# Performance work log

Measured on AMD Instinct MI355X. Metric: run time of the kernel, lower is better.

## Reference

```python
import jax, jax.numpy as jnp
import numpy as np

N = 20000
E = 320000
IN_CH = 512
OUT_CH = 256


def setup_inputs() -> dict:
    key = jax.random.key(0)
    ks = jax.random.split(key, 24)
    p = lambda k, shape: jax.random.normal(k, shape, jnp.float32) * 0.05
    return {
        "x": jax.random.normal(ks[0], (N, IN_CH), jnp.float32),
        "edge_index": jax.random.randint(ks[1], (2, E), 0, N),
        "original_size": 16384,
        "W1": p(ks[2], (IN_CH, 4 * 256)), "as1": p(ks[3], (4, 256)), "ad1": p(ks[4], (4, 256)), "b1": p(ks[5], (1024,)),
        "lw1": p(ks[6], (IN_CH, 1024)), "lb1": p(ks[7], (1024,)),
        "W2": p(ks[8], (1024, 4 * 256)), "as2": p(ks[9], (4, 256)), "ad2": p(ks[10], (4, 256)), "b2": p(ks[11], (1024,)),
        "lw2": p(ks[12], (1024, 1024)), "lb2": p(ks[13], (1024,)),
        "W3": p(ks[14], (1024, 6 * 256)), "as3": p(ks[15], (6, 256)), "ad3": p(ks[16], (6, 256)), "b3": p(ks[17], (256,)),
        "lw3": p(ks[18], (1024, OUT_CH)), "lb3": p(ks[19], (OUT_CH,)),
    }


def gat_conv(x, src, dst, W, a_src, a_dst, bias, heads, ch, concat):
    """PyG-style GATConv: gather -> edge attention -> segment softmax -> scatter-add."""
    n = x.shape[0]
    h = (x @ W).reshape(n, heads, ch)                      # [N,H,C]
    alpha_s = (h * a_src[None]).sum(-1)                    # [N,H]
    alpha_d = (h * a_dst[None]).sum(-1)                    # [N,H]
    e = jax.nn.leaky_relu(alpha_s[src] + alpha_d[dst], 0.2)  # [E,H]
    m = jax.ops.segment_max(e, dst, num_segments=n)        # per-dst max (stable softmax)
    e = jnp.exp(e - m[dst])
    denom = jax.ops.segment_sum(e, dst, num_segments=n)
    alpha = e / (denom[dst] + 1e-16)                       # [E,H]
    msg = h[src] * alpha[:, :, None]                       # [E,H,C]
    out = jax.ops.segment_sum(msg, dst, num_segments=n)    # [N,H,C]
    out = out.reshape(n, heads * ch) if concat else out.mean(axis=1)
    return out + bias


def reference(x, edge_index, original_size, W1, as1, ad1, b1, lw1, lb1,
              W2, as2, ad2, b2, lw2, lb2, W3, as3, ad3, b3, lw3, lb3):
    n = x.shape[0]
    loops = jnp.arange(n)
    src = jnp.concatenate([edge_index[0], loops])  # PyG add_self_loops=True default
    dst = jnp.concatenate([edge_index[1], loops])
    h = jax.nn.elu(gat_conv(x, src, dst, W1, as1, ad1, b1, 4, 256, True) + x @ lw1 + lb1)
    h = jax.nn.elu(gat_conv(h, src, dst, W2, as2, ad2, b2, 4, 256, True) + h @ lw2 + lb2)
    h = gat_conv(h, src, dst, W3, as3, ad3, b3, 6, 256, False) + h @ lw3 + lb3
    return h[:original_size]
```

## Files before the change

### kernel.cpp

```cpp
#include <hip/hip_runtime.h>

#define N_NODES 20000
#define M_PAD   20096
#define E_EDGES 320000

typedef unsigned short u16;
typedef unsigned int   u32;
typedef __attribute__((ext_vector_type(8))) short bf16x8;
typedef __attribute__((ext_vector_type(4))) float f32x4;

__device__ __forceinline__ float bf2f(u16 u){
  u32 x = ((u32)u) << 16; float f; __builtin_memcpy(&f, &x, 4); return f;
}
__device__ __forceinline__ u16 f2bf(float f){
  u32 u; __builtin_memcpy(&u, &f, 4);
  u += 0x7fffu + ((u >> 16) & 1u);
  return (u16)(u >> 16);
}

__device__ __forceinline__ void gl_lds16(const void* g, void* l){
  __builtin_amdgcn_global_load_lds((const __attribute__((address_space(1))) void*)g,
                                   (__attribute__((address_space(3))) void*)l, 16, 0, 0);
}

__global__ void hist_k(const int* __restrict__ ei, int* __restrict__ cnt){
  int i = blockIdx.x * 256 + threadIdx.x;
  if (i < E_EDGES) atomicAdd(&cnt[ei[E_EDGES + i]], 1);
}

__global__ void scan_k(const int* __restrict__ cnt, int* __restrict__ rowp, int n){
  __shared__ int buf[1024]; __shared__ int carry;
  int tid = threadIdx.x;
  if (tid == 0) carry = 0;
  __syncthreads();
  for (int base = 0; base < n; base += 1024){
    int i = base + tid;
    int v = (i < n) ? cnt[i] : 0;
    buf[tid] = v; __syncthreads();
    for (int off = 1; off < 1024; off <<= 1){
      int t = (tid >= off) ? buf[tid - off] : 0; __syncthreads();
      buf[tid] += t; __syncthreads();
    }
    int incl = buf[tid];
    int c0 = carry;
    __syncthreads();
    if (i < n) rowp[i] = c0 + incl - v;
    if (tid == 1023) carry = c0 + incl;
    __syncthreads();
  }
  if (tid == 0) rowp[n] = carry;
}

__global__ void copy_int_k(const int* __restrict__ a, int* __restrict__ b, int n){
  int i = blockIdx.x * 256 + threadIdx.x; if (i < n) b[i] = a[i];
}

__global__ void scatter_k(const int* __restrict__ ei, int* __restrict__ fill, int* __restrict__ esrc){
  int i = blockIdx.x * 256 + threadIdx.x;
  if (i < E_EDGES){
    int d = ei[E_EDGES + i];
    int p = atomicAdd(&fill[d], 1);
    esrc[p] = ei[i];
  }
}

__global__ void tcast_k(const float* __restrict__ src, int Nc, u16* __restrict__ dst, int n0, int ldd){
  __shared__ float tile[32][33];
  int kb = blockIdx.y * 32, nb = blockIdx.x * 32;
  int tx = threadIdx.x, ty = threadIdx.y;
#pragma unroll
  for (int r = 0; r < 32; r += 8)
    tile[ty + r][tx] = src[(size_t)(kb + ty + r) * Nc + nb + tx];
  __syncthreads();
#pragma unroll
  for (int r = 0; r < 32; r += 8){
    int n = nb + ty + r;
    dst[(size_t)(n0 + n) * ldd + kb + tx] = f2bf(tile[tx][ty + r]);
  }
}

__global__ void castx_k(const float* __restrict__ x, u16* __restrict__ o, int realRows, int cols){
  int r = blockIdx.y, c = blockIdx.x * 256 + threadIdx.x;
  float v = (r < realRows) ? x[(size_t)r * cols + c] : 0.f;
  o[(size_t)r * cols + c] = f2bf(v);
}

__global__ void zpad_k(u16* __restrict__ p, int n){
  int i = blockIdx.x * 256 + threadIdx.x; if (i < n) p[i] = 0;
}

__global__ __launch_bounds__(256)
void gemm_bf16(const u16* __restrict__ A, const u16* __restrict__ Bt, u16* __restrict__ C,
               int N, int K)
{
  __shared__ __attribute__((aligned(16))) u16 lA[128 * 32];
  __shared__ __attribute__((aligned(16))) u16 lB[128 * 32];
  const int tid  = threadIdx.x;
  const int wave = tid >> 6, lane = tid & 63;
  const int bm = blockIdx.x, bn = blockIdx.y;
  const int wm = (wave >> 1) * 64, wn = (wave & 1) * 64;

  const int srow  = wave * 16 + (lane >> 2);
  const int skcol = (lane & 3) * 8;
  const u16* Ag0 = A  + (size_t)(bm * 128 + srow) * K + skcol;
  const u16* Ag1 = Ag0 + (size_t)64 * K;
  const u16* Bg0 = Bt + (size_t)(bn * 128 + srow) * K + skcol;
  const u16* Bg1 = Bg0 + (size_t)64 * K;
  u16* lA0 = lA + wave * 512; u16* lA1 = lA + 2048 + wave * 512;
  u16* lB0 = lB + wave * 512; u16* lB1 = lB + 2048 + wave * 512;

  f32x4 acc[4][4] = {};

  for (int k0 = 0; k0 < K; k0 += 32){
    gl_lds16(Ag0 + k0, lA0);
    gl_lds16(Ag1 + k0, lA1);
    gl_lds16(Bg0 + k0, lB0);
    gl_lds16(Bg1 + k0, lB1);
    __syncthreads();
    const int koff = (lane >> 4) * 8;
    const int rsel = lane & 15;
    bf16x8 af[4], bfr[4];
#pragma unroll
    for (int i = 0; i < 4; i++) af[i]  = *(const bf16x8*)&lA[(wm + i * 16 + rsel) * 32 + koff];
#pragma unroll
    for (int j = 0; j < 4; j++) bfr[j] = *(const bf16x8*)&lB[(wn + j * 16 + rsel) * 32 + koff];
#pragma unroll
    for (int i = 0; i < 4; i++)
#pragma unroll
      for (int j = 0; j < 4; j++)
        acc[i][j] = __builtin_amdgcn_mfma_f32_16x16x32_bf16(af[i], bfr[j], acc[i][j], 0, 0, 0);
    __syncthreads();
  }

  const int r0 = (lane >> 4) * 4, cl = lane & 15;
#pragma unroll
  for (int i = 0; i < 4; i++)
#pragma unroll
    for (int j = 0; j < 4; j++){
      int row = bm * 128 + wm + i * 16 + r0;
      int col = bn * 128 + wn + j * 16 + cl;
      u16* cp = C + (size_t)row * N + col;
#pragma unroll
      for (int r = 0; r < 4; r++) cp[(size_t)r * N] = f2bf(acc[i][j][r]);
    }
}

__global__ void alpha_k(const u16* __restrict__ HG, int ldH,
                        const float* __restrict__ a_s, const float* __restrict__ a_d,
                        float* __restrict__ aS, float* __restrict__ aD, int H)
{
  int n = blockIdx.x, h = blockIdx.y, lane = threadIdx.x;
  const u16* rp = HG + (size_t)n * ldH + h * 256 + lane * 4;
  ushort4 u = *(const ushort4*)rp;
  float4 av = *(const float4*)(a_s + h * 256 + lane * 4);
  float4 dv = *(const float4*)(a_d + h * 256 + lane * 4);
  float x0 = bf2f(u.x), x1 = bf2f(u.y), x2 = bf2f(u.z), x3 = bf2f(u.w);
  float s = x0 * av.x + x1 * av.y + x2 * av.z + x3 * av.w;
  float d = x0 * dv.x + x1 * dv.y + x2 * dv.z + x3 * dv.w;
#pragma unroll
  for (int off = 32; off; off >>= 1){ s += __shfl_down(s, off); d += __shfl_down(d, off); }
  if (lane == 0){ aS[(size_t)n * H + h] = s; aD[(size_t)n * H + h] = d; }
}

template<int H, bool FINAL>
__global__ __launch_bounds__(256)
void agg_k(const u16* __restrict__ HG, int ldH,
           const int* __restrict__ rowp, const int* __restrict__ esrc,
           const float* __restrict__ aS, const float* __restrict__ aD,
           const float* __restrict__ bias, const float* __restrict__ lbias,
           int gatCols, u16* __restrict__ outb, int ldo, float* __restrict__ outf)
{
  constexpr int PERT = H;
  constexpr int MAXE = 256;
  __shared__ float s_m[H], s_dinv[H], s_red[4 * H];
  __shared__ float s_ew[MAXE * H];
  __shared__ float s_fin[FINAL ? 1536 : 4];

  const int dst = blockIdx.x;
  const int tid = threadIdx.x, lane = tid & 63, wv = tid >> 6;
  const int e0 = rowp[dst];
  const int deg = rowp[dst + 1] - e0;
  const int nE = deg + 1;

  float adv[H];
#pragma unroll
  for (int h = 0; h < H; h++) adv[h] = aD[(size_t)dst * H + h];

  float lm[H];
#pragma unroll
  for (int h = 0; h < H; h++) lm[h] = -1e30f;
  for (int i = tid; i < nE; i += 256){
    int s = (i == deg) ? dst : esrc[e0 + i];
#pragma unroll
    for (int h = 0; h < H; h++){
      float e = aS[(size_t)s * H + h] + adv[h];
      e = e > 0.f ? e : 0.2f * e;
      lm[h] = fmaxf(lm[h], e);
    }
  }
#pragma unroll
  for (int h = 0; h < H; h++)
#pragma unroll
    for (int off = 32; off; off >>= 1) lm[h] = fmaxf(lm[h], __shfl_down(lm[h], off));
  if (lane == 0){
#pragma unroll
    for (int h = 0; h < H; h++) s_red[wv * H + h] = lm[h];
  }
  __syncthreads();
  if (tid < H) s_m[tid] = fmaxf(fmaxf(s_red[tid], s_red[H + tid]),
                                fmaxf(s_red[2 * H + tid], s_red[3 * H + tid]));
  __syncthreads();

  float ls[H];
#pragma unroll
  for (int h = 0; h < H; h++) ls[h] = 0.f;
  for (int i = tid; i < nE; i += 256){
    int s = (i == deg) ? dst : esrc[e0 + i];
#pragma unroll
    for (int h = 0; h < H; h++){
      float e = aS[(size_t)s * H + h] + adv[h];
      e = e > 0.f ? e : 0.2f * e;
      float w = __expf(e - s_m[h]);
      if (i < MAXE) s_ew[i * H + h] = w;
      ls[h] += w;
    }
  }
#pragma unroll
  for (int h = 0; h < H; h++)
#pragma unroll
    for (int off = 32; off; off >>= 1) ls[h] += __shfl_down(ls[h], off);
  if (lane == 0){
#pragma unroll
    for (int h = 0; h < H; h++) s_red[wv * H + h] = ls[h];
  }
  __syncthreads();
  if (tid < H) s_dinv[tid] = 1.f / (s_red[tid] + s_red[H + tid] + s_red[2 * H + tid] + s_red[3 * H + tid] + 1e-16f);
  __syncthreads();

  float acc[PERT];
#pragma unroll
  for (int c = 0; c < PERT; c++) acc[c] = 0.f;
  const int ch0 = tid * PERT;

  if constexpr (H == 4){
    const int hh = tid >> 6;
    const float dinv = s_dinv[hh];
    for (int i = 0; i < nE; i++){
      int s = (i == deg) ? dst : esrc[e0 + i];
      float w;
      if (i < MAXE) w = s_ew[i * 4 + hh];
      else {
        float e = aS[(size_t)s * 4 + hh] + aD[(size_t)dst * 4 + hh];
        e = e > 0.f ? e : 0.2f * e;
        w = __expf(e - s_m[hh]);
      }
      float cfc = w * dinv;
      const u16* rp = HG + (size_t)s * ldH;
      ushort4 u = *(const ushort4*)(rp + ch0);
      acc[0] += cfc * bf2f(u.x); acc[1] += cfc * bf2f(u.y);
      acc[2] += cfc * bf2f(u.z); acc[3] += cfc * bf2f(u.w);
    }
  } else {
    const int h0 = ch0 >> 8;
    const int h1 = (ch0 + 5) >> 8;
    const float dinv0 = s_dinv[h0], dinv1 = s_dinv[h1];
    const int bnd = (h0 + 1) * 256;
    for (int i = 0; i < nE; i++){
      int s = (i == deg) ? dst : esrc[e0 + i];
      float w0, w1;
      if (i < MAXE){ w0 = s_ew[i * 6 + h0]; w1 = s_ew[i * 6 + h1]; }
      else {
        float ea = aS[(size_t)s * 6 + h0] + aD[(size_t)dst * 6 + h0];
        ea = ea > 0.f ? ea : 0.2f * ea;
        w0 = __expf(ea - s_m[h0]);
        float eb = aS[(size_t)s * 6 + h1] + aD[(size_t)dst * 6 + h1];
        eb = eb > 0.f ? eb : 0.2f * eb;
        w1 = __expf(eb - s_m[h1]);
      }
      float c0 = w0 * dinv0, c1 = w1 * dinv1;
      const u32* rp4 = (const u32*)(HG + (size_t)s * ldH);
      u32 u0 = rp4[tid * 3], u1 = rp4[tid * 3 + 1], u2 = rp4[tid * 3 + 2];
      float v[6] = { bf2f((u16)(u0 & 0xffff)), bf2f((u16)(u0 >> 16)),
                     bf2f((u16)(u1 & 0xffff)), bf2f((u16)(u1 >> 16)),
                     bf2f((u16)(u2 & 0xffff)), bf2f((u16)(u2 >> 16)) };
#pragma unroll
      for (int c = 0; c < 6; c++) acc[c] += ((ch0 + c) < bnd ? c0 : c1) * v[c];
    }
  }

  if constexpr (FINAL){
#pragma unroll
    for (int c = 0; c < PERT; c++) s_fin[ch0 + c] = acc[c];
    __syncthreads();
    int c = tid;
    float v = 0.f;
#pragma unroll
    for (int h = 0; h < 6; h++) v += s_fin[h * 256 + c];
    v = v * (1.f / 6.f) + bias[c] + bf2f(HG[(size_t)dst * ldH + gatCols + c]) + lbias[c];
    outf[(size_t)dst * 256 + c] = v;
  } else {
    const u16* lr = HG + (size_t)dst * ldH + gatCols;
    ushort4 u = *(const ushort4*)(lr + ch0);
    float lv[4] = { bf2f(u.x), bf2f(u.y), bf2f(u.z), bf2f(u.w) };
    ushort4 o;
    float v0 = acc[0] + bias[ch0 + 0] + lv[0] + lbias[ch0 + 0]; v0 = v0 > 0.f ? v0 : __expf(v0) - 1.f;
    float v1 = acc[1] + bias[ch0 + 1] + lv[1] + lbias[ch0 + 1]; v1 = v1 > 0.f ? v1 : __expf(v1) - 1.f;
    float v2 = acc[2] + bias[ch0 + 2] + lv[2] + lbias[ch0 + 2]; v2 = v2 > 0.f ? v2 : __expf(v2) - 1.f;
    float v3 = acc[3] + bias[ch0 + 3] + lv[3] + lbias[ch0 + 3]; v3 = v3 > 0.f ? v3 : __expf(v3) - 1.f;
    o.x = f2bf(v0); o.y = f2bf(v1); o.z = f2bf(v2); o.w = f2bf(v3);
    *(ushort4*)(outb + (size_t)dst * ldo + ch0) = o;
  }
}

extern "C" void kernel_launch(void* const* d_in, const int* in_sizes, int n_in,
                              void* d_out, int out_size, void* d_ws, size_t ws_size,
                              hipStream_t stream)
{
  const float* x   = (const float*)d_in[0];
  const int*   ei  = (const int*)  d_in[1];
  const float* W1  = (const float*)d_in[3];
  const float* as1 = (const float*)d_in[4];
  const float* ad1 = (const float*)d_in[5];
  const float* b1  = (const float*)d_in[6];
  const float* lw1 = (const float*)d_in[7];
  const float* lb1 = (const float*)d_in[8];
  const float* W2  = (const float*)d_in[9];
  const float* as2 = (const float*)d_in[10];
  const float* ad2 = (const float*)d_in[11];
  const float* b2  = (const float*)d_in[12];
  const float* lw2 = (const float*)d_in[13];
  const float* lb2 = (const float*)d_in[14];
  const float* W3  = (const float*)d_in[15];
  const float* as3 = (const float*)d_in[16];
  const float* ad3 = (const float*)d_in[17];
  const float* b3  = (const float*)d_in[18];
  const float* lw3 = (const float*)d_in[19];
  const float* lb3 = (const float*)d_in[20];

  char* wp = (char*)d_ws;
  auto nxt = [&](size_t b) -> void* {
    void* p = (void*)wp; wp += (b + 255) & ~(size_t)255; return p;
  };
  u16*  Wt1  = (u16*) nxt((size_t)2048 * 512  * 2);
  u16*  Wt2  = (u16*) nxt((size_t)2048 * 1024 * 2);
  u16*  Wt3  = (u16*) nxt((size_t)1792 * 1024 * 2);
  u16*  Xb   = (u16*) nxt((size_t)M_PAD * 1024 * 2);
  u16*  HG   = (u16*) nxt((size_t)M_PAD * 2048 * 2);
  float* aS  = (float*)nxt((size_t)N_NODES * 6 * 4);
  float* aD  = (float*)nxt((size_t)N_NODES * 6 * 4);
  int*  cnt  = (int*)  nxt((size_t)N_NODES * 4);
  int*  rowp = (int*)  nxt((size_t)(N_NODES + 1) * 4);
  int*  fill = (int*)  nxt((size_t)N_NODES * 4);
  int*  esrc = (int*)  nxt((size_t)E_EDGES * 4);

  hipMemsetAsync(cnt, 0, (size_t)N_NODES * 4, stream);
  hist_k   <<<(E_EDGES + 255) / 256, 256, 0, stream>>>(ei, cnt);
  scan_k   <<<1, 1024, 0, stream>>>(cnt, rowp, N_NODES);
  copy_int_k<<<(N_NODES + 255) / 256, 256, 0, stream>>>(rowp, fill, N_NODES);
  scatter_k<<<(E_EDGES + 255) / 256, 256, 0, stream>>>(ei, fill, esrc);

  dim3 tb(32, 8);
  tcast_k<<<dim3(1024 / 32, 512  / 32), tb, 0, stream>>>(W1,  1024, Wt1, 0,    512);
  tcast_k<<<dim3(1024 / 32, 512  / 32), tb, 0, stream>>>(lw1, 1024, Wt1, 1024, 512);
  tcast_k<<<dim3(1024 / 32, 1024 / 32), tb, 0, stream>>>(W2,  1024, Wt2, 0,    1024);
  tcast_k<<<dim3(1024 / 32, 1024 / 32), tb, 0, stream>>>(lw2, 1024, Wt2, 1024, 1024);
  tcast_k<<<dim3(1536 / 32, 1024 / 32), tb, 0, stream>>>(W3,  1536, Wt3, 0,    1024);
  tcast_k<<<dim3(256  / 32, 1024 / 32), tb, 0, stream>>>(lw3, 256,  Wt3, 1536, 1024);

  castx_k<<<dim3(512 / 256, M_PAD), 256, 0, stream>>>(x, Xb, N_NODES, 512);
  zpad_k <<<(96 * 1024 + 255) / 256, 256, 0, stream>>>(Xb + (size_t)N_NODES * 1024, 96 * 1024);

  const int MT = M_PAD / 128;

  gemm_bf16<<<dim3(MT, 2048 / 128), 256, 0, stream>>>(Xb, Wt1, HG, 2048, 512);
  alpha_k  <<<dim3(N_NODES, 4), 64, 0, stream>>>(HG, 2048, as1, ad1, aS, aD, 4);
  agg_k<4, false><<<N_NODES, 256, 0, stream>>>(HG, 2048, rowp, esrc, aS, aD, b1, lb1, 1024, Xb, 1024, nullptr);

  gemm_bf16<<<dim3(MT, 2048 / 128), 256, 0, stream>>>(Xb, Wt2, HG, 2048, 1024);
  alpha_k  <<<dim3(N_NODES, 4), 64, 0, stream>>>(HG, 2048, as2, ad2, aS, aD, 4);
  agg_k<4, false><<<N_NODES, 256, 0, stream>>>(HG, 2048, rowp, esrc, aS, aD, b2, lb2, 1024, Xb, 1024, nullptr);

  gemm_bf16<<<dim3(MT, 1792 / 128), 256, 0, stream>>>(Xb, Wt3, HG, 1792, 1024);
  alpha_k  <<<dim3(N_NODES, 6), 64, 0, stream>>>(HG, 1792, as3, ad3, aS, aD, 6);
  int outRows = out_size / 256;
  agg_k<6, true><<<outRows, 256, 0, stream>>>(HG, 1792, rowp, esrc, aS, aD, b3, lb3, 1536, nullptr, 0, (float*)d_out);

  (void)in_sizes; (void)n_in; (void)ws_size;
}
```

Baseline: 962.2 us.

## Widen GEMM tile, cache edge scores in LDS, and use wave-level scan

The GEMM tile grows from 128x128 to 128x256, so each block holds twice as many accumulators. The grid is reordered so N-tiles vary fastest, which lets blocks share A rows in cache. The aggregation kernel stores source indices and leaky-relu scores in LDS during the max pass, so the exp pass and the gather loop no longer reload esrc and aS. The gather loop is also unrolled by two edges. The scan now uses wave shuffles instead of a barrier-heavy LDS scan, and castx writes packed pairs. The wider tile raises register pressure and could lower occupancy.

```diff
diff --git a/kernel.cpp b/kernel.cpp
--- a/kernel.cpp
+++ b/kernel.cpp
@@ -29,25 +29,32 @@
 }
 
 __global__ void scan_k(const int* __restrict__ cnt, int* __restrict__ rowp, int n){
-  __shared__ int buf[1024]; __shared__ int carry;
-  int tid = threadIdx.x;
+  __shared__ int wsum[16], wpre[16];
+  __shared__ int carry;
+  int tid = threadIdx.x, lane = tid & 63, wv = tid >> 6;
   if (tid == 0) carry = 0;
   __syncthreads();
   for (int base = 0; base < n; base += 1024){
     int i = base + tid;
     int v = (i < n) ? cnt[i] : 0;
-    buf[tid] = v; __syncthreads();
-    for (int off = 1; off < 1024; off <<= 1){
-      int t = (tid >= off) ? buf[tid - off] : 0; __syncthreads();
-      buf[tid] += t; __syncthreads();
-    }
-    int incl = buf[tid];
-    int c0 = carry;
+    int incl = v;
+#pragma unroll
+    for (int d = 1; d < 64; d <<= 1){
+      int t = __shfl_up(incl, d, 64);
+      if (lane >= d) incl += t;
+    }
+    if (lane == 63) wsum[wv] = incl;
     __syncthreads();
-    if (i < n) rowp[i] = c0 + incl - v;
-    if (tid == 1023) carry = c0 + incl;
+    if (tid == 0){
+      int s = carry;
+#pragma unroll
+      for (int w = 0; w < 16; w++){ wpre[w] = s; s += wsum[w]; }
+      carry = s;
+    }
     __syncthreads();
-  }
+    if (i < n) rowp[i] = wpre[wv] + incl - v;
+  }
+  __syncthreads();
   if (tid == 0) rowp[n] = carry;
 }
 
@@ -79,55 +86,56 @@
   }
 }
 
-__global__ void castx_k(const float* __restrict__ x, u16* __restrict__ o, int realRows, int cols){
-  int r = blockIdx.y, c = blockIdx.x * 256 + threadIdx.x;
-  float v = (r < realRows) ? x[(size_t)r * cols + c] : 0.f;
-  o[(size_t)r * cols + c] = f2bf(v);
+__global__ void castx_k(const float* __restrict__ x, u16* __restrict__ o, int realRows){
+  int r = blockIdx.x, c = threadIdx.x * 2;
+  float2 v = (r < realRows) ? *(const float2*)(x + (size_t)r * 512 + c) : make_float2(0.f, 0.f);
+  u32 pk = ((u32)f2bf(v.y) << 16) | (u32)f2bf(v.x);
+  *(u32*)(o + (size_t)r * 512 + c) = pk;
 }
 
 __global__ void zpad_k(u16* __restrict__ p, int n){
   int i = blockIdx.x * 256 + threadIdx.x; if (i < n) p[i] = 0;
 }
 
-__global__ __launch_bounds__(256)
+__global__ __launch_bounds__(256, 2)
 void gemm_bf16(const u16* __restrict__ A, const u16* __restrict__ Bt, u16* __restrict__ C,
                int N, int K)
 {
   __shared__ __attribute__((aligned(16))) u16 lA[128 * 32];
-  __shared__ __attribute__((aligned(16))) u16 lB[128 * 32];
+  __shared__ __attribute__((aligned(16))) u16 lB[256 * 32];
   const int tid  = threadIdx.x;
   const int wave = tid >> 6, lane = tid & 63;
-  const int bm = blockIdx.x, bn = blockIdx.y;
-  const int wm = (wave >> 1) * 64, wn = (wave & 1) * 64;
+  const int bn = blockIdx.x, bm = blockIdx.y;
+  const int wm = (wave >> 1) * 64, wn = (wave & 1) * 128;
 
   const int srow  = wave * 16 + (lane >> 2);
   const int skcol = (lane & 3) * 8;
   const u16* Ag0 = A  + (size_t)(bm * 128 + srow) * K + skcol;
   const u16* Ag1 = Ag0 + (size_t)64 * K;
-  const u16* Bg0 = Bt + (size_t)(bn * 128 + srow) * K + skcol;
-  const u16* Bg1 = Bg0 + (size_t)64 * K;
+  const u16* Bg  = Bt + (size_t)(bn * 256 + srow) * K + skcol;
   u16* lA0 = lA + wave * 512; u16* lA1 = lA + 2048 + wave * 512;
-  u16* lB0 = lB + wave * 512; u16* lB1 = lB + 2048 + wave * 512;
-
-  f32x4 acc[4][4] = {};
+  u16* lBw = lB + wave * 512;
+
+  f32x4 acc[4][8] = {};
 
   for (int k0 = 0; k0 < K; k0 += 32){
     gl_lds16(Ag0 + k0, lA0);
     gl_lds16(Ag1 + k0, lA1);
-    gl_lds16(Bg0 + k0, lB0);
-    gl_lds16(Bg1 + k0, lB1);
+#pragma unroll
+    for (int c = 0; c < 4; c++)
+      gl_lds16(Bg + (size_t)(c * 64) * K + k0, lBw + c * 2048);
     __syncthreads();
     const int koff = (lane >> 4) * 8;
     const int rsel = lane & 15;
-    bf16x8 af[4], bfr[4];
+    bf16x8 af[4], bfr[8];
 #pragma unroll
     for (int i = 0; i < 4; i++) af[i]  = *(const bf16x8*)&lA[(wm + i * 16 + rsel) * 32 + koff];
 #pragma unroll
-    for (int j = 0; j < 4; j++) bfr[j] = *(const bf16x8*)&lB[(wn + j * 16 + rsel) * 32 + koff];
+    for (int j = 0; j < 8; j++) bfr[j] = *(const bf16x8*)&lB[(wn + j * 16 + rsel) * 32 + koff];
 #pragma unroll
     for (int i = 0; i < 4; i++)
 #pragma unroll
-      for (int j = 0; j < 4; j++)
+      for (int j = 0; j < 8; j++)
         acc[i][j] = __builtin_amdgcn_mfma_f32_16x16x32_bf16(af[i], bfr[j], acc[i][j], 0, 0, 0);
     __syncthreads();
   }
@@ -136,9 +144,9 @@
 #pragma unroll
   for (int i = 0; i < 4; i++)
 #pragma unroll
-    for (int j = 0; j < 4; j++){
+    for (int j = 0; j < 8; j++){
       int row = bm * 128 + wm + i * 16 + r0;
-      int col = bn * 128 + wn + j * 16 + cl;
+      int col = bn * 256 + wn + j * 16 + cl;
       u16* cp = C + (size_t)row * N + col;
 #pragma unroll
       for (int r = 0; r < 4; r++) cp[(size_t)r * N] = f2bf(acc[i][j][r]);
@@ -171,9 +179,10 @@
            int gatCols, u16* __restrict__ outb, int ldo, float* __restrict__ outf)
 {
   constexpr int PERT = H;
-  constexpr int MAXE = 256;
+  constexpr int MAXE = 320;
   __shared__ float s_m[H], s_dinv[H], s_red[4 * H];
   __shared__ float s_ew[MAXE * H];
+  __shared__ int   s_src[MAXE];
   __shared__ float s_fin[FINAL ? 1536 : 4];
 
   const int dst = blockIdx.x;
@@ -181,6 +190,7 @@
   const int e0 = rowp[dst];
   const int deg = rowp[dst + 1] - e0;
   const int nE = deg + 1;
+  const bool fits = (nE <= MAXE);
 
   float adv[H];
 #pragma unroll
@@ -191,10 +201,12 @@
   for (int h = 0; h < H; h++) lm[h] = -1e30f;
   for (int i = tid; i < nE; i += 256){
     int s = (i == deg) ? dst : esrc[e0 + i];
+    if (fits) s_src[i] = s;
 #pragma unroll
     for (int h = 0; h < H; h++){
       float e = aS[(size_t)s * H + h] + adv[h];
       e = e > 0.f ? e : 0.2f * e;
+      if (fits) s_ew[i * H + h] = e;
       lm[h] = fmaxf(lm[h], e);
     }
   }
@@ -215,14 +227,21 @@
 #pragma unroll
   for (int h = 0; h < H; h++) ls[h] = 0.f;
   for (int i = tid; i < nE; i += 256){
-    int s = (i == deg) ? dst : esrc[e0 + i];
-#pragma unroll
-    for (int h = 0; h < H; h++){
-      float e = aS[(size_t)s * H + h] + adv[h];
-      e = e > 0.f ? e : 0.2f * e;
-      float w = __expf(e - s_m[h]);
-      if (i < MAXE) s_ew[i * H + h] = w;
-      ls[h] += w;
+    if (fits){
+#pragma unroll
+      for (int h = 0; h < H; h++){
+        float w = __expf(s_ew[i * H + h] - s_m[h]);
+        s_ew[i * H + h] = w;
+        ls[h] += w;
+      }
+    } else {
+      int s = (i == deg) ? dst : esrc[e0 + i];
+#pragma unroll
+      for (int h = 0; h < H; h++){
+        float e = aS[(size_t)s * H + h] + adv[h];
+        e = e > 0.f ? e : 0.2f * e;
+        ls[h] += __expf(e - s_m[h]);
+      }
     }
   }
 #pragma unroll
@@ -245,46 +264,95 @@
   if constexpr (H == 4){
     const int hh = tid >> 6;
     const float dinv = s_dinv[hh];
-    for (int i = 0; i < nE; i++){
-      int s = (i == deg) ? dst : esrc[e0 + i];
-      float w;
-      if (i < MAXE) w = s_ew[i * 4 + hh];
-      else {
-        float e = aS[(size_t)s * 4 + hh] + aD[(size_t)dst * 4 + hh];
+    const u16* HGb = HG + ch0;
+    if (fits){
+      int i = 0;
+      for (; i + 2 <= nE; i += 2){
+        int s0 = s_src[i], s1 = s_src[i + 1];
+        float w0 = s_ew[i * 4 + hh] * dinv;
+        float w1 = s_ew[i * 4 + 4 + hh] * dinv;
+        ushort4 u0 = *(const ushort4*)(HGb + (size_t)s0 * ldH);
+        ushort4 u1 = *(const ushort4*)(HGb + (size_t)s1 * ldH);
+        acc[0] += w0 * bf2f(u0.x) + w1 * bf2f(u1.x);
+        acc[1] += w0 * bf2f(u0.y) + w1 * bf2f(u1.y);
+        acc[2] += w0 * bf2f(u0.z) + w1 * bf2f(u1.z);
+        acc[3] += w0 * bf2f(u0.w) + w1 * bf2f(u1.w);
+      }
+      if (i < nE){
+        int s0 = s_src[i];
+        float w0 = s_ew[i * 4 + hh] * dinv;
+        ushort4 u0 = *(const ushort4*)(HGb + (size_t)s0 * ldH);
+        acc[0] += w0 * bf2f(u0.x); acc[1] += w0 * bf2f(u0.y);
+        acc[2] += w0 * bf2f(u0.z); acc[3] += w0 * bf2f(u0.w);
+      }
+    } else {
+      for (int i = 0; i < nE; i++){
+        int s = (i == deg) ? dst : esrc[e0 + i];
+        float e = aS[(size_t)s * 4 + hh] + adv[hh];
         e = e > 0.f ? e : 0.2f * e;
-        w = __expf(e - s_m[hh]);
-      }
-      float cfc = w * dinv;
-      const u16* rp = HG + (size_t)s * ldH;
-      ushort4 u = *(const ushort4*)(rp + ch0);
-      acc[0] += cfc * bf2f(u.x); acc[1] += cfc * bf2f(u.y);
-      acc[2] += cfc * bf2f(u.z); acc[3] += cfc * bf2f(u.w);
+        float w = __expf(e - s_m[hh]) * dinv;
+        ushort4 u = *(const ushort4*)(HGb + (size_t)s * ldH);
+        acc[0] += w * bf2f(u.x); acc[1] += w * bf2f(u.y);
+        acc[2] += w * bf2f(u.z); acc[3] += w * bf2f(u.w);
+      }
     }
   } else {
     const int h0 = ch0 >> 8;
     const int h1 = (ch0 + 5) >> 8;
     const float dinv0 = s_dinv[h0], dinv1 = s_dinv[h1];
     const int bnd = (h0 + 1) * 256;
-    for (int i = 0; i < nE; i++){
-      int s = (i == deg) ? dst : esrc[e0 + i];
-      float w0, w1;
-      if (i < MAXE){ w0 = s_ew[i * 6 + h0]; w1 = s_ew[i * 6 + h1]; }
-      else {
-        float ea = aS[(size_t)s * 6 + h0] + aD[(size_t)dst * 6 + h0];
+    const u32* HGb = (const u32*)HG;
+    const int rowd = ldH >> 1;
+    if (fits){
+      int i = 0;
+      for (; i + 2 <= nE; i += 2){
+        int s0 = s_src[i], s1 = s_src[i + 1];
+        float p0 = s_ew[i * 6 + h0] * dinv0, q0 = s_ew[i * 6 + h1] * dinv1;
+        float p1 = s_ew[i * 6 + 6 + h0] * dinv0, q1 = s_ew[i * 6 + 6 + h1] * dinv1;
+        const u32* r0p = HGb + (size_t)s0 * rowd + tid * 3;
+        const u32* r1p = HGb + (size_t)s1 * rowd + tid * 3;
+        u32 a0 = r0p[0], a1 = r0p[1], a2 = r0p[2];
+        u32 b0 = r1p[0], b1 = r1p[1], b2 = r1p[2];
+        float v0[6] = { bf2f((u16)(a0 & 0xffff)), bf2f((u16)(a0 >> 16)),
+                        bf2f((u16)(a1 & 0xffff)), bf2f((u16)(a1 >> 16)),
+                        bf2f((u16)(a2 & 0xffff)), bf2f((u16)(a2 >> 16)) };
+        float v1[6] = { bf2f((u16)(b0 & 0xffff)), bf2f((u16)(b0 >> 16)),
+                        bf2f((u16)(b1 & 0xffff)), bf2f((u16)(b1 >> 16)),
+                        bf2f((u16)(b2 & 0xffff)), bf2f((u16)(b2 >> 16)) };
+#pragma unroll
+        for (int c = 0; c < 6; c++){
+          bool lo = (ch0 + c) < bnd;
+          acc[c] += (lo ? p0 : q0) * v0[c] + (lo ? p1 : q1) * v1[c];
+        }
+      }
+      if (i < nE){
+        int s0 = s_src[i];
+        float p0 = s_ew[i * 6 + h0] * dinv0, q0 = s_ew[i * 6 + h1] * dinv1;
+        const u32* r0p = HGb + (size_t)s0 * rowd + tid * 3;
+        u32 a0 = r0p[0], a1 = r0p[1], a2 = r0p[2];
+        float v0[6] = { bf2f((u16)(a0 & 0xffff)), bf2f((u16)(a0 >> 16)),
+                        bf2f((u16)(a1 & 0xffff)), bf2f((u16)(a1 >> 16)),
+                        bf2f((u16)(a2 & 0xffff)), bf2f((u16)(a2 >> 16)) };
+#pragma unroll
+        for (int c = 0; c < 6; c++) acc[c] += (((ch0 + c) < bnd) ? p0 : q0) * v0[c];
+      }
+    } else {
+      for (int i = 0; i < nE; i++){
+        int s = (i == deg) ? dst : esrc[e0 + i];
+        float ea = aS[(size_t)s * 6 + h0] + adv[h0];
         ea = ea > 0.f ? ea : 0.2f * ea;
-        w0 = __expf(ea - s_m[h0]);
-        float eb = aS[(size_t)s * 6 + h1] + aD[(size_t)dst * 6 + h1];
+        float p0 = __expf(ea - s_m[h0]) * dinv0;
+        float eb = aS[(size_t)s * 6 + h1] + adv[h1];
         eb = eb > 0.f ? eb : 0.2f * eb;
-        w1 = __expf(eb - s_m[h1]);
-      }
-      float c0 = w0 * dinv0, c1 = w1 * dinv1;
-      const u32* rp4 = (const u32*)(HG + (size_t)s * ldH);
-      u32 u0 = rp4[tid * 3], u1 = rp4[tid * 3 + 1], u2 = rp4[tid * 3 + 2];
-      float v[6] = { bf2f((u16)(u0 & 0xffff)), bf2f((u16)(u0 >> 16)),
-                     bf2f((u16)(u1 & 0xffff)), bf2f((u16)(u1 >> 16)),
-                     bf2f((u16)(u2 & 0xffff)), bf2f((u16)(u2 >> 16)) };
-#pragma unroll
-      for (int c = 0; c < 6; c++) acc[c] += ((ch0 + c) < bnd ? c0 : c1) * v[c];
+        float q0 = __expf(eb - s_m[h1]) * dinv1;
+        const u32* r0p = HGb + (size_t)s * rowd + tid * 3;
+        u32 a0 = r0p[0], a1 = r0p[1], a2 = r0p[2];
+        float v0[6] = { bf2f((u16)(a0 & 0xffff)), bf2f((u16)(a0 >> 16)),
+                        bf2f((u16)(a1 & 0xffff)), bf2f((u16)(a1 >> 16)),
+                        bf2f((u16)(a2 & 0xffff)), bf2f((u16)(a2 >> 16)) };
+#pragma unroll
+        for (int c = 0; c < 6; c++) acc[c] += (((ch0 + c) < bnd) ? p0 : q0) * v0[c];
+      }
     }
   }
 
@@ -367,20 +435,20 @@
   tcast_k<<<dim3(1536 / 32, 1024 / 32), tb, 0, stream>>>(W3,  1536, Wt3, 0,    1024);
   tcast_k<<<dim3(256  / 32, 1024 / 32), tb, 0, stream>>>(lw3, 256,  Wt3, 1536, 1024);
 
-  castx_k<<<dim3(512 / 256, M_PAD), 256, 0, stream>>>(x, Xb, N_NODES, 512);
+  castx_k<<<M_PAD, 256, 0, stream>>>(x, Xb, N_NODES);
   zpad_k <<<(96 * 1024 + 255) / 256, 256, 0, stream>>>(Xb + (size_t)N_NODES * 1024, 96 * 1024);
 
   const int MT = M_PAD / 128;
 
-  gemm_bf16<<<dim3(MT, 2048 / 128), 256, 0, stream>>>(Xb, Wt1, HG, 2048, 512);
+  gemm_bf16<<<dim3(2048 / 256, MT), 256, 0, stream>>>(Xb, Wt1, HG, 2048, 512);
   alpha_k  <<<dim3(N_NODES, 4), 64, 0, stream>>>(HG, 2048, as1, ad1, aS, aD, 4);
   agg_k<4, false><<<N_NODES, 256, 0, stream>>>(HG, 2048, rowp, esrc, aS, aD, b1, lb1, 1024, Xb, 1024, nullptr);
 
-  gemm_bf16<<<dim3(MT, 2048 / 128), 256, 0, stream>>>(Xb, Wt2, HG, 2048, 1024);
+  gemm_bf16<<<dim3(2048 / 256, MT), 256, 0, stream>>>(Xb, Wt2, HG, 2048, 1024);
   alpha_k  <<<dim3(N_NODES, 4), 64, 0, stream>>>(HG, 2048, as2, ad2, aS, aD, 4);
   agg_k<4, false><<<N_NODES, 256, 0, stream>>>(HG, 2048, rowp, esrc, aS, aD, b2, lb2, 1024, Xb, 1024, nullptr);
 
-  gemm_bf16<<<dim3(MT, 1792 / 128), 256, 0, stream>>>(Xb, Wt3, HG, 1792, 1024);
+  gemm_bf16<<<dim3(1792 / 256, MT), 256, 0, stream>>>(Xb, Wt3, HG, 1792, 1024);
   alpha_k  <<<dim3(N_NODES, 6), 64, 0, stream>>>(HG, 1792, as3, ad3, aS, aD, 6);
   int outRows = out_size / 256;
   agg_k<6, true><<<outRows, 256, 0, stream>>>(HG, 1792, rowp, esrc, aS, aD, b3, lb3, 1536, nullptr, 0, (float*)d_out);
```

After: 909.1 us. 5.5% less time.
